# Optimization experiments

Measured on AMD Instinct MI355X. Metric: run time of the kernel, lower is better.

The kernel has to match this reference:

```python
import jax, jax.numpy as jnp
import numpy as np

NUM_ENT_CLASS = 150
NORMED_REL_VEC_DIST = False


def box_cxcywh_to_xyxy(b):
    cx, cy, w, h = b[..., 0], b[..., 1], b[..., 2], b[..., 3]
    return jnp.stack([cx - 0.5 * w, cy - 0.5 * h, cx + 0.5 * w, cy + 0.5 * h], axis=-1)


def box_xyxy_to_cxcywh(b):
    x0, y0, x1, y1 = b[..., 0], b[..., 1], b[..., 2], b[..., 3]
    return jnp.stack([(x0 + x1) * 0.5, (y0 + y1) * 0.5, x1 - x0, y1 - y0], axis=-1)


def generalized_box_iou(a, b):
    # a: [N,4], b: [M,4], xyxy -> [N,M]
    area_a = (a[:, 2] - a[:, 0]) * (a[:, 3] - a[:, 1])
    area_b = (b[:, 2] - b[:, 0]) * (b[:, 3] - b[:, 1])
    lt = jnp.maximum(a[:, None, :2], b[None, :, :2])
    rb = jnp.minimum(a[:, None, 2:], b[None, :, 2:])
    wh = jnp.clip(rb - lt, 0.0)
    inter = wh[..., 0] * wh[..., 1]
    union = area_a[:, None] + area_b[None, :] - inter
    iou = inter / union
    lt_c = jnp.minimum(a[:, None, :2], b[None, :, :2])
    rb_c = jnp.maximum(a[:, None, 2:], b[None, :, 2:])
    wh_c = jnp.clip(rb_c - lt_c, 0.0)
    area_c = wh_c[..., 0] * wh_c[..., 1]
    return iou - (area_c - union) / area_c


def cdist_l2(a, b):
    # a: [N,C], b: [M,C] -> [N,M] euclidean distance (gram-matrix form)
    d2 = (jnp.sum(a * a, -1)[:, None] + jnp.sum(b * b, -1)[None, :]
          - 2.0 * (a @ b.T))
    return jnp.sqrt(jnp.maximum(d2, 1e-12))


def _per_image(ent_box_n, ent_logits, ro_logits, rs_logits, ro_box_n, rs_box_n,
               rel_vec_n, scale):
    # scale: [4] = [w, h, w, h]
    ent_box = box_cxcywh_to_xyxy(ent_box_n) * scale[None, :]           # [Ne,4] pixels
    ent_cnter = box_xyxy_to_cxcywh(ent_box)[..., :2]                    # [Ne,2]
    ent_cnter_normed = ent_box_n[..., :2]

    # num_ent_class (150) != logits dim (151) -> softmax, drop background
    ro_dist = jax.nn.softmax(ro_logits, axis=-1)[..., :-1]              # [Nr,150]
    rs_dist = jax.nn.softmax(rs_logits, axis=-1)[..., :-1]
    ent_prob = jax.nn.softmax(ent_logits, axis=-1)[..., :-1]            # [Ne,150]
    ent_score = jnp.max(ent_prob, axis=-1)                              # [Ne]

    ro_box = box_cxcywh_to_xyxy(ro_box_n) * scale[None, :]              # [Nr,4]
    rs_box = box_cxcywh_to_xyxy(rs_box_n) * scale[None, :]
    rel_vec = rel_vec_n * scale[None, :]                                # [Nr,4]

    if NORMED_REL_VEC_DIST:
        vec, sc, oc = rel_vec_n, ent_cnter_normed, ent_cnter_normed
    else:
        vec, sc, oc = rel_vec, ent_cnter, ent_cnter

    # L1 distance of rel-vector endpoints to entity centers -> [Nr,Ne]
    dist_s = (jnp.abs(vec[:, None, 0] - sc[None, :, 0])
              + jnp.abs(vec[:, None, 1] - sc[None, :, 1]))
    dist_o = (jnp.abs(vec[:, None, 2] - oc[None, :, 0])
              + jnp.abs(vec[:, None, 3] - oc[None, :, 1]))
    match_vec_sub = 1.0 / (dist_s + 1.0)
    match_vec_obj = 1.0 / (dist_o + 1.0)

    m_s = ent_score[None, :] * match_vec_sub                            # conf-weighted
    m_o = ent_score[None, :] * match_vec_obj

    sub_giou = jnp.clip(generalized_box_iou(ent_box, rs_box), 0.0)      # [Ne,Nr]
    obj_giou = jnp.clip(generalized_box_iou(ent_box, ro_box), 0.0)

    sub_cls = 1.0 / (cdist_l2(rs_dist, ent_prob) + 1.0)                 # [Nr,Ne]
    obj_cls = 1.0 / (cdist_l2(ro_dist, ent_prob) + 1.0)

    dist_s_final = m_s * sub_cls * sub_giou.T                           # [Nr,Ne]
    dist_o_final = m_o * obj_cls * obj_giou.T
    return dist_s_final, dist_o_final


def setup_inputs() -> dict:
    key = jax.random.key(0)
    ks = jax.random.split(key, 8)
    B, Ne, Nr, C1 = 64, 500, 500, NUM_ENT_CLASS + 1
    inp = {
        "pred_boxes": jax.random.uniform(ks[0], (B, Ne, 4), jnp.float32),
        "pred_logits": jax.random.normal(ks[1], (B, Ne, C1), jnp.float32),
        "pred_rel_obj_logits": jax.random.normal(ks[2], (B, Nr, C1), jnp.float32),
        "pred_rel_sub_logits": jax.random.normal(ks[3], (B, Nr, C1), jnp.float32),
        "pred_rel_obj_box": jax.random.uniform(ks[4], (B, Nr, 4), jnp.float32),
        "pred_rel_sub_box": jax.random.uniform(ks[5], (B, Nr, 4), jnp.float32),
        "pred_rel_vec": jax.random.uniform(ks[6], (B, Nr, 4), jnp.float32),
        "target_sizes": 600.0 + 600.0 * jax.random.uniform(ks[7], (B, 2), jnp.float32),
    }
    return inp


def reference(pred_boxes, pred_logits, pred_rel_obj_logits, pred_rel_sub_logits,
              pred_rel_obj_box, pred_rel_sub_box, pred_rel_vec, target_sizes):
    img_h, img_w = target_sizes[:, 0], target_sizes[:, 1]
    scale_fct = jnp.stack([img_w, img_h, img_w, img_h], axis=1)  # [B,4]
    sub_dist, obj_dist = jax.vmap(_per_image)(
        pred_boxes, pred_logits, pred_rel_obj_logits, pred_rel_sub_logits,
        pred_rel_obj_box, pred_rel_sub_box, pred_rel_vec, scale_fct)
    return sub_dist, obj_dist
```

## Files before the change

kernel.cpp:

```cpp
#include <hip/hip_runtime.h>
#include <math.h>

#define NB   64
#define NPT  500
#define NPTP 512
#define C1   151
#define CM1  150
#define KP   160
#define EAF  12
#define RAF  20

typedef __bf16 bf16x8 __attribute__((ext_vector_type(8)));
typedef float  f32x4  __attribute__((ext_vector_type(4)));

__device__ __forceinline__ float rcpf(float x) { return __builtin_amdgcn_rcpf(x); }
__device__ __forceinline__ float rsqf(float x) { return __builtin_amdgcn_rsqf(x); }

extern "C" __global__ void __launch_bounds__(256)
k_pre(const float* __restrict__ boxes, const float* __restrict__ ent_logits,
      const float* __restrict__ ro_logits, const float* __restrict__ rs_logits,
      const float* __restrict__ ro_box, const float* __restrict__ rs_box,
      const float* __restrict__ rel_vec, const float* __restrict__ tsz,
      __bf16* __restrict__ entP, __bf16* __restrict__ rsP, __bf16* __restrict__ roP,
      float* __restrict__ entAux, float* __restrict__ relAux)
{
    const int w    = threadIdx.x >> 6;
    const int lane = threadIdx.x & 63;
    const int row  = blockIdx.x * 4 + w;
    const int set  = row / (NB * NPT);
    const int idx  = row - set * (NB * NPT);
    const int b    = idx / NPT;
    const int i    = idx - b * NPT;

    const float* src = (set == 0 ? ent_logits : (set == 1 ? rs_logits : ro_logits))
                       + (size_t)(b * NPT + i) * C1;

    const float x0 = src[lane];
    const float x1 = src[lane + 64];
    const float x2 = (lane < C1 - 128) ? src[lane + 128] : -INFINITY;

    float m = fmaxf(fmaxf(x0, x1), x2);
    #pragma unroll
    for (int off = 32; off; off >>= 1) m = fmaxf(m, __shfl_xor(m, off, 64));

    const float e0 = __expf(x0 - m);
    const float e1 = __expf(x1 - m);
    const float e2 = (lane < C1 - 128) ? __expf(x2 - m) : 0.f;
    float s = e0 + e1 + e2;
    #pragma unroll
    for (int off = 32; off; off >>= 1) s += __shfl_xor(s, off, 64);

    const float inv = 1.f / s;
    const float p0 = e0 * inv;
    const float p1 = e1 * inv;
    const float p2 = e2 * inv;

    __bf16* dst = (set == 0 ? entP : (set == 1 ? rsP : roP)) + ((size_t)b * NPTP + i) * KP;
    dst[lane]      = (__bf16)p0;
    dst[lane + 64] = (__bf16)p1;
    if (lane + 128 < KP)
        dst[lane + 128] = (lane + 128 < CM1) ? (__bf16)p2 : (__bf16)0.f;

    float pm = fmaxf(p0, p1);
    float nn = p0 * p0 + p1 * p1;
    if (lane + 128 < CM1) { pm = fmaxf(pm, p2); nn += p2 * p2; }
    #pragma unroll
    for (int off = 32; off; off >>= 1) {
        pm = fmaxf(pm, __shfl_xor(pm, off, 64));
        nn += __shfl_xor(nn, off, 64);
    }

    if (lane == 0) {
        const float hh = tsz[b * 2 + 0];
        const float ww = tsz[b * 2 + 1];
        if (set == 0) {
            const float* bb = boxes + (size_t)(b * NPT + i) * 4;
            const float cx = bb[0], cy = bb[1], bw = bb[2], bh = bb[3];
            const float X0 = (cx - 0.5f * bw) * ww, Y0 = (cy - 0.5f * bh) * hh;
            const float X1 = (cx + 0.5f * bw) * ww, Y1 = (cy + 0.5f * bh) * hh;
            float* A = entAux + (size_t)(b * NPT + i) * EAF;
            A[0] = pm;
            A[1] = 0.5f * (X0 + X1);
            A[2] = 0.5f * (Y0 + Y1);
            A[3] = nn;
            A[4] = X0; A[5] = Y0; A[6] = X1; A[7] = Y1;
            A[8] = (X1 - X0) * (Y1 - Y0);
        } else if (set == 1) {
            const float* bb = rs_box  + (size_t)(b * NPT + i) * 4;
            const float* vv = rel_vec + (size_t)(b * NPT + i) * 4;
            const float cx = bb[0], cy = bb[1], bw = bb[2], bh = bb[3];
            float* A = relAux + (size_t)(b * NPT + i) * RAF;
            const float X0 = (cx - 0.5f * bw) * ww, Y0 = (cy - 0.5f * bh) * hh;
            const float X1 = (cx + 0.5f * bw) * ww, Y1 = (cy + 0.5f * bh) * hh;
            A[0] = X0; A[1] = Y0; A[2] = X1; A[3] = Y1;
            A[8]  = vv[0] * ww; A[9]  = vv[1] * hh;
            A[10] = vv[2] * ww; A[11] = vv[3] * hh;
            A[12] = nn;
            A[14] = (X1 - X0) * (Y1 - Y0);
        } else {
            const float* bb = ro_box + (size_t)(b * NPT + i) * 4;
            const float cx = bb[0], cy = bb[1], bw = bb[2], bh = bb[3];
            float* A = relAux + (size_t)(b * NPT + i) * RAF;
            const float X0 = (cx - 0.5f * bw) * ww, Y0 = (cy - 0.5f * bh) * hh;
            const float X1 = (cx + 0.5f * bw) * ww, Y1 = (cy + 0.5f * bh) * hh;
            A[4] = X0; A[5] = Y0; A[6] = X1; A[7] = Y1;
            A[13] = nn;
            A[15] = (X1 - X0) * (Y1 - Y0);
        }
    }
}

template <bool FULL>
__device__ __forceinline__ void epilogue(
    const float (*eA)[EAF], const float (*rA)[RAF],
    const f32x4* accS, const f32x4* accO,
    int lr, int kq, int wv, int b, int e0T, int r0T,
    float* __restrict__ outS, float* __restrict__ outO)
{
    f32x4 ev0[4], ev1[4];
    float eArea[4];
    #pragma unroll
    for (int et = 0; et < 4; ++et) {
        const float* ep = eA[et * 16 + lr];
        ev0[et] = *(const f32x4*)(ep);
        ev1[et] = *(const f32x4*)(ep + 4);
        eArea[et] = ep[8];
    }

    const unsigned baseR0 = ((unsigned)b * NPT + (unsigned)(r0T + wv * 16 + kq * 4)) * NPT;
    const unsigned eBase  = (unsigned)(e0T + lr);

    #pragma unroll
    for (int reg = 0; reg < 4; ++reg) {
        const int rIdx = wv * 16 + kq * 4 + reg;
        const bool rOK = FULL || (r0T + rIdx < NPT);
        const float* rp = rA[rIdx];
        const f32x4 rsB = *(const f32x4*)(rp);
        const f32x4 roB = *(const f32x4*)(rp + 4);
        const f32x4 vv  = *(const f32x4*)(rp + 8);
        const f32x4 rn  = *(const f32x4*)(rp + 12);
        const unsigned rowOff = baseR0 + (unsigned)reg * NPT;

        #pragma unroll
        for (int et = 0; et < 4; ++et) {
            const float score = ev0[et][0], ecx = ev0[et][1], ecy = ev0[et][2], en2 = ev0[et][3];
            const float ex0 = ev1[et][0], ey0 = ev1[et][1], ex1 = ev1[et][2], ey1 = ev1[et][3];
            const float aE = eArea[et];

            const float iwS = fmaxf(fminf(ex1, rsB[2]) - fmaxf(ex0, rsB[0]), 0.f);
            const float ihS = fmaxf(fminf(ey1, rsB[3]) - fmaxf(ey0, rsB[1]), 0.f);
            const float inS = iwS * ihS;
            const float unS = aE + rn[2] - inS;
            const float aCS = (fmaxf(ex1, rsB[2]) - fminf(ex0, rsB[0]))
                            * (fmaxf(ey1, rsB[3]) - fminf(ey0, rsB[1]));
            const float gS  = fmaxf(fmaf(inS, rcpf(unS), fmaf(unS, rcpf(aCS), -1.f)), 0.f);

            const float iwO = fmaxf(fminf(ex1, roB[2]) - fmaxf(ex0, roB[0]), 0.f);
            const float ihO = fmaxf(fminf(ey1, roB[3]) - fmaxf(ey0, roB[1]), 0.f);
            const float inO = iwO * ihO;
            const float unO = aE + rn[3] - inO;
            const float aCO = (fmaxf(ex1, roB[2]) - fminf(ex0, roB[0]))
                            * (fmaxf(ey1, roB[3]) - fminf(ey0, roB[1]));
            const float gO  = fmaxf(fmaf(inO, rcpf(unO), fmaf(unO, rcpf(aCO), -1.f)), 0.f);

            const float d2s = fmaxf(fmaf(-2.f, accS[et][reg], rn[0] + en2), 1e-12f);
            const float d2o = fmaxf(fmaf(-2.f, accO[et][reg], rn[1] + en2), 1e-12f);
            const float dS  = d2s * rsqf(d2s);
            const float dO  = d2o * rsqf(d2o);
            const float distS = fabsf(vv[0] - ecx) + fabsf(vv[1] - ecy);
            const float distO = fabsf(vv[2] - ecx) + fabsf(vv[3] - ecy);
            const float qS = rcpf((distS + 1.f) * (dS + 1.f));
            const float qO = rcpf((distO + 1.f) * (dO + 1.f));

            const float vS = score * qS * gS;
            const float vO = score * qO * gO;

            const unsigned o = rowOff + eBase + (unsigned)(et * 16);
            if (FULL || (rOK && (int)(eBase + et * 16) < NPT)) {
                outS[o] = vS;
                outO[o] = vO;
            }
        }
    }
}

extern "C" __global__ void __launch_bounds__(256, 4)
k_main(const __bf16* __restrict__ entP, const __bf16* __restrict__ rsP,
       const __bf16* __restrict__ roP, const float* __restrict__ eAuxG,
       const float* __restrict__ rAuxG,
       float* __restrict__ outS, float* __restrict__ outO)
{
    __shared__ __align__(16) float eA[64][EAF];
    __shared__ __align__(16) float rA[64][RAF];

    const int tid = threadIdx.x;
    const int b   = blockIdx.z;
    const int e0T = blockIdx.x * 64;
    const int r0T = blockIdx.y * 64;

    {
        const float4 z = {0.f, 0.f, 0.f, 0.f};
        for (int t = tid; t < 64 * (EAF / 4); t += 256) {
            const int e = t / (EAF / 4), q = t % (EAF / 4);
            const int ge = e0T + e;
            ((float4*)eA[e])[q] = (ge < NPT)
                ? ((const float4*)(eAuxG + ((size_t)b * NPT + ge) * EAF))[q] : z;
        }
        for (int t = tid; t < 64 * (RAF / 4); t += 256) {
            const int r = t / (RAF / 4), q = t % (RAF / 4);
            const int gr = r0T + r;
            ((float4*)rA[r])[q] = (gr < NPT)
                ? ((const float4*)(rAuxG + ((size_t)b * NPT + gr) * RAF))[q] : z;
        }
    }
    __syncthreads();

    const int wv   = tid >> 6;
    const int lane = tid & 63;
    const int lr   = lane & 15;
    const int kq   = lane >> 4;

    const size_t bOff = (size_t)b * NPTP;
    const __bf16* rsRow = rsP  + (bOff + r0T + wv * 16 + lr) * KP;
    const __bf16* roRow = roP  + (bOff + r0T + wv * 16 + lr) * KP;
    const __bf16* enRow = entP + (bOff + e0T + lr) * KP;

    f32x4 accS[4] = {{0,0,0,0},{0,0,0,0},{0,0,0,0},{0,0,0,0}};
    f32x4 accO[4] = {{0,0,0,0},{0,0,0,0},{0,0,0,0},{0,0,0,0}};

    #pragma unroll
    for (int ks = 0; ks < 5; ++ks) {
        const int ko = ks * 32 + kq * 8;
        const bf16x8 ars = *(const bf16x8*)(rsRow + ko);
        const bf16x8 aro = *(const bf16x8*)(roRow + ko);
        #pragma unroll
        for (int et = 0; et < 4; ++et) {
            const bf16x8 be = *(const bf16x8*)(enRow + (size_t)et * 16 * KP + ko);
            accS[et] = __builtin_amdgcn_mfma_f32_16x16x32_bf16(ars, be, accS[et], 0, 0, 0);
            accO[et] = __builtin_amdgcn_mfma_f32_16x16x32_bf16(aro, be, accO[et], 0, 0, 0);
        }
    }

    if (e0T + 64 <= NPT && r0T + 64 <= NPT) {
        epilogue<true >(eA, rA, accS, accO, lr, kq, wv, b, e0T, r0T, outS, outO);
    } else {
        epilogue<false>(eA, rA, accS, accO, lr, kq, wv, b, e0T, r0T, outS, outO);
    }
}

extern "C" void kernel_launch(void* const* d_in, const int* in_sizes, int n_in,
                              void* d_out, int out_size, void* d_ws, size_t ws_size,
                              hipStream_t stream)
{
    const float* boxes      = (const float*)d_in[0];
    const float* ent_logits = (const float*)d_in[1];
    const float* ro_logits  = (const float*)d_in[2];
    const float* rs_logits  = (const float*)d_in[3];
    const float* ro_box     = (const float*)d_in[4];
    const float* rs_box     = (const float*)d_in[5];
    const float* rel_vec    = (const float*)d_in[6];
    const float* tsz        = (const float*)d_in[7];

    const size_t PROB_ELEMS = (size_t)NB * NPTP * KP;
    __bf16* entP = (__bf16*)d_ws;
    __bf16* rsP  = entP + PROB_ELEMS;
    __bf16* roP  = rsP  + PROB_ELEMS;
    float*  eAux = (float*)(roP + PROB_ELEMS);
    float*  rAux = eAux + (size_t)NB * NPT * EAF;

    float* outS = (float*)d_out;
    float* outO = outS + (size_t)NB * NPT * NPT;

    hipLaunchKernelGGL(k_pre, dim3(24000), dim3(256), 0, stream,
                       boxes, ent_logits, ro_logits, rs_logits,
                       ro_box, rs_box, rel_vec, tsz,
                       entP, rsP, roP, eAux, rAux);

    hipLaunchKernelGGL(k_main, dim3(8, 8, NB), dim3(256), 0, stream,
                       entP, rsP, roP, eAux, rAux, outS, outO);
}
```

Baseline: 276.0 us.

## Use 16-lane rows in softmax prep and MFMA-fragment probability layout

The prep kernel now handles one row per 16 lanes instead of per wavefront, which cuts the number of blocks and shuffle rounds. It computes the max probability and squared norm from the exp values, with no second reduction pass. Probabilities are written in a grouped layout that matches the MFMA operand fragments, so each lane's bf16x8 loads in the main kernel are contiguous across lanes. The main grid also puts the batch index first, likely to improve L2 locality between tiles of the same image. In exchange, the stores in the prep kernel become scattered 2-byte writes.

After: 235.7 us. 1.17x faster.

```diff
diff --git a/kernel.cpp b/kernel.cpp
--- a/kernel.cpp
+++ b/kernel.cpp
@@ -3,12 +3,14 @@
 
 #define NB   64
 #define NPT  500
-#define NPTP 512
 #define C1   151
 #define CM1  150
-#define KP   160
 #define EAF  12
 #define RAF  20
+
+#define GRP_ELEMS  2560
+#define IMG_ELEMS  (32 * GRP_ELEMS)
+#define PROB_ELEMS ((size_t)NB * IMG_ELEMS)
 
 typedef __bf16 bf16x8 __attribute__((ext_vector_type(8)));
 typedef float  f32x4  __attribute__((ext_vector_type(4)));
@@ -24,61 +26,76 @@
       __bf16* __restrict__ entP, __bf16* __restrict__ rsP, __bf16* __restrict__ roP,
       float* __restrict__ entAux, float* __restrict__ relAux)
 {
-    const int w    = threadIdx.x >> 6;
-    const int lane = threadIdx.x & 63;
-    const int row  = blockIdx.x * 4 + w;
-    const int set  = row / (NB * NPT);
-    const int idx  = row - set * (NB * NPT);
-    const int b    = idx / NPT;
-    const int i    = idx - b * NPT;
+    const int tid = threadIdx.x;
+    const int q   = tid & 15;
+    const int rl  = tid >> 4;
+    const int bx  = blockIdx.x;
+    const int set = bx / 2000;
+    const int rowIdx = (bx - set * 2000) * 16 + rl;
+    const int b = rowIdx / 500;
+    const int i = rowIdx - b * 500;
 
     const float* src = (set == 0 ? ent_logits : (set == 1 ? rs_logits : ro_logits))
-                       + (size_t)(b * NPT + i) * C1;
-
-    const float x0 = src[lane];
-    const float x1 = src[lane + 64];
-    const float x2 = (lane < C1 - 128) ? src[lane + 128] : -INFINITY;
-
-    float m = fmaxf(fmaxf(x0, x1), x2);
-    #pragma unroll
-    for (int off = 32; off; off >>= 1) m = fmaxf(m, __shfl_xor(m, off, 64));
-
-    const float e0 = __expf(x0 - m);
-    const float e1 = __expf(x1 - m);
-    const float e2 = (lane < C1 - 128) ? __expf(x2 - m) : 0.f;
-    float s = e0 + e1 + e2;
-    #pragma unroll
-    for (int off = 32; off; off >>= 1) s += __shfl_xor(s, off, 64);
-
-    const float inv = 1.f / s;
-    const float p0 = e0 * inv;
-    const float p1 = e1 * inv;
-    const float p2 = e2 * inv;
-
-    __bf16* dst = (set == 0 ? entP : (set == 1 ? rsP : roP)) + ((size_t)b * NPTP + i) * KP;
-    dst[lane]      = (__bf16)p0;
-    dst[lane + 64] = (__bf16)p1;
-    if (lane + 128 < KP)
-        dst[lane + 128] = (lane + 128 < CM1) ? (__bf16)p2 : (__bf16)0.f;
-
-    float pm = fmaxf(p0, p1);
-    float nn = p0 * p0 + p1 * p1;
-    if (lane + 128 < CM1) { pm = fmaxf(pm, p2); nn += p2 * p2; }
-    #pragma unroll
-    for (int off = 32; off; off >>= 1) {
-        pm = fmaxf(pm, __shfl_xor(pm, off, 64));
-        nn += __shfl_xor(nn, off, 64);
-    }
-
-    if (lane == 0) {
+                       + (size_t)rowIdx * C1;
+
+    float x[10];
+    #pragma unroll
+    for (int t = 0; t < 9; ++t) x[t] = src[q + 16 * t];
+    x[9] = (q <= 6) ? src[q + 144] : -INFINITY;
+
+    float mAll = x[0];
+    #pragma unroll
+    for (int t = 1; t < 10; ++t) mAll = fmaxf(mAll, x[t]);
+    float mKept = x[0];
+    #pragma unroll
+    for (int t = 1; t < 9; ++t) mKept = fmaxf(mKept, x[t]);
+    if (q <= 5) mKept = fmaxf(mKept, x[9]);
+
+    #pragma unroll
+    for (int off = 1; off < 16; off <<= 1) {
+        mAll  = fmaxf(mAll,  __shfl_xor(mAll,  off, 16));
+        mKept = fmaxf(mKept, __shfl_xor(mKept, off, 16));
+    }
+
+    float e[10], s = 0.f, s2 = 0.f;
+    #pragma unroll
+    for (int t = 0; t < 9; ++t) {
+        e[t] = __expf(x[t] - mAll);
+        s  += e[t];
+        s2 += e[t] * e[t];
+    }
+    e[9] = (q <= 6) ? __expf(x[9] - mAll) : 0.f;
+    s += e[9];
+    if (q <= 5) s2 += e[9] * e[9];
+
+    #pragma unroll
+    for (int off = 1; off < 16; off <<= 1) {
+        s  += __shfl_xor(s,  off, 16);
+        s2 += __shfl_xor(s2, off, 16);
+    }
+
+    const float inv = rcpf(s);
+    const float pm  = __expf(mKept - mAll) * inv;
+    const float nn  = s2 * inv * inv;
+
+    __bf16* dstT = (set == 0 ? entP : (set == 1 ? rsP : roP));
+    const int g  = i >> 4, ir = i & 15;
+    __bf16* dst = dstT + ((size_t)b * 32 + g) * GRP_ELEMS + ir * 8 + (q & 7);
+    const int qh = q >> 3;
+    #pragma unroll
+    for (int t = 0; t < 9; ++t)
+        dst[(2 * t + qh) * 128] = (__bf16)(e[t] * inv);
+    dst[(18 + qh) * 128] = (q <= 5) ? (__bf16)(e[9] * inv) : (__bf16)0.f;
+
+    if (q == 0) {
         const float hh = tsz[b * 2 + 0];
         const float ww = tsz[b * 2 + 1];
         if (set == 0) {
-            const float* bb = boxes + (size_t)(b * NPT + i) * 4;
+            const float* bb = boxes + (size_t)rowIdx * 4;
             const float cx = bb[0], cy = bb[1], bw = bb[2], bh = bb[3];
             const float X0 = (cx - 0.5f * bw) * ww, Y0 = (cy - 0.5f * bh) * hh;
             const float X1 = (cx + 0.5f * bw) * ww, Y1 = (cy + 0.5f * bh) * hh;
-            float* A = entAux + (size_t)(b * NPT + i) * EAF;
+            float* A = entAux + (size_t)rowIdx * EAF;
             A[0] = pm;
             A[1] = 0.5f * (X0 + X1);
             A[2] = 0.5f * (Y0 + Y1);
@@ -86,10 +103,10 @@
             A[4] = X0; A[5] = Y0; A[6] = X1; A[7] = Y1;
             A[8] = (X1 - X0) * (Y1 - Y0);
         } else if (set == 1) {
-            const float* bb = rs_box  + (size_t)(b * NPT + i) * 4;
-            const float* vv = rel_vec + (size_t)(b * NPT + i) * 4;
+            const float* bb = rs_box  + (size_t)rowIdx * 4;
+            const float* vv = rel_vec + (size_t)rowIdx * 4;
             const float cx = bb[0], cy = bb[1], bw = bb[2], bh = bb[3];
-            float* A = relAux + (size_t)(b * NPT + i) * RAF;
+            float* A = relAux + (size_t)rowIdx * RAF;
             const float X0 = (cx - 0.5f * bw) * ww, Y0 = (cy - 0.5f * bh) * hh;
             const float X1 = (cx + 0.5f * bw) * ww, Y1 = (cy + 0.5f * bh) * hh;
             A[0] = X0; A[1] = Y0; A[2] = X1; A[3] = Y1;
@@ -98,9 +115,9 @@
             A[12] = nn;
             A[14] = (X1 - X0) * (Y1 - Y0);
         } else {
-            const float* bb = ro_box + (size_t)(b * NPT + i) * 4;
+            const float* bb = ro_box + (size_t)rowIdx * 4;
             const float cx = bb[0], cy = bb[1], bw = bb[2], bh = bb[3];
-            float* A = relAux + (size_t)(b * NPT + i) * RAF;
+            float* A = relAux + (size_t)rowIdx * RAF;
             const float X0 = (cx - 0.5f * bw) * ww, Y0 = (cy - 0.5f * bh) * hh;
             const float X1 = (cx + 0.5f * bw) * ww, Y1 = (cy + 0.5f * bh) * hh;
             A[4] = X0; A[5] = Y0; A[6] = X1; A[7] = Y1;
@@ -194,23 +211,23 @@
     __shared__ __align__(16) float rA[64][RAF];
 
     const int tid = threadIdx.x;
-    const int b   = blockIdx.z;
-    const int e0T = blockIdx.x * 64;
-    const int r0T = blockIdx.y * 64;
+    const int b   = blockIdx.x;
+    const int e0T = (blockIdx.y & 7) * 64;
+    const int r0T = (blockIdx.y >> 3) * 64;
 
     {
         const float4 z = {0.f, 0.f, 0.f, 0.f};
         for (int t = tid; t < 64 * (EAF / 4); t += 256) {
-            const int e = t / (EAF / 4), q = t % (EAF / 4);
+            const int e = t / (EAF / 4), qq = t % (EAF / 4);
             const int ge = e0T + e;
-            ((float4*)eA[e])[q] = (ge < NPT)
-                ? ((const float4*)(eAuxG + ((size_t)b * NPT + ge) * EAF))[q] : z;
+            ((float4*)eA[e])[qq] = (ge < NPT)
+                ? ((const float4*)(eAuxG + ((size_t)b * NPT + ge) * EAF))[qq] : z;
         }
         for (int t = tid; t < 64 * (RAF / 4); t += 256) {
-            const int r = t / (RAF / 4), q = t % (RAF / 4);
+            const int r = t / (RAF / 4), qq = t % (RAF / 4);
             const int gr = r0T + r;
-            ((float4*)rA[r])[q] = (gr < NPT)
-                ? ((const float4*)(rAuxG + ((size_t)b * NPT + gr) * RAF))[q] : z;
+            ((float4*)rA[r])[qq] = (gr < NPT)
+                ? ((const float4*)(rAuxG + ((size_t)b * NPT + gr) * RAF))[qq] : z;
         }
     }
     __syncthreads();
@@ -220,22 +237,23 @@
     const int lr   = lane & 15;
     const int kq   = lane >> 4;
 
-    const size_t bOff = (size_t)b * NPTP;
-    const __bf16* rsRow = rsP  + (bOff + r0T + wv * 16 + lr) * KP;
-    const __bf16* roRow = roP  + (bOff + r0T + wv * 16 + lr) * KP;
-    const __bf16* enRow = entP + (bOff + e0T + lr) * KP;
+    const int gR = (r0T >> 4) + wv;
+    const int gE = (e0T >> 4);
+    const __bf16* rsBase = rsP  + ((size_t)b * 32 + gR) * GRP_ELEMS + lr * 8;
+    const __bf16* roBase = roP  + ((size_t)b * 32 + gR) * GRP_ELEMS + lr * 8;
+    const __bf16* enBase = entP + ((size_t)b * 32 + gE) * GRP_ELEMS + lr * 8;
 
     f32x4 accS[4] = {{0,0,0,0},{0,0,0,0},{0,0,0,0},{0,0,0,0}};
     f32x4 accO[4] = {{0,0,0,0},{0,0,0,0},{0,0,0,0},{0,0,0,0}};
 
     #pragma unroll
     for (int ks = 0; ks < 5; ++ks) {
-        const int ko = ks * 32 + kq * 8;
-        const bf16x8 ars = *(const bf16x8*)(rsRow + ko);
-        const bf16x8 aro = *(const bf16x8*)(roRow + ko);
+        const int kOff = (ks * 4 + kq) * 128;
+        const bf16x8 ars = *(const bf16x8*)(rsBase + kOff);
+        const bf16x8 aro = *(const bf16x8*)(roBase + kOff);
         #pragma unroll
         for (int et = 0; et < 4; ++et) {
-            const bf16x8 be = *(const bf16x8*)(enRow + (size_t)et * 16 * KP + ko);
+            const bf16x8 be = *(const bf16x8*)(enBase + et * GRP_ELEMS + kOff);
             accS[et] = __builtin_amdgcn_mfma_f32_16x16x32_bf16(ars, be, accS[et], 0, 0, 0);
             accO[et] = __builtin_amdgcn_mfma_f32_16x16x32_bf16(aro, be, accO[et], 0, 0, 0);
         }
@@ -261,7 +279,6 @@
     const float* rel_vec    = (const float*)d_in[6];
     const float* tsz        = (const float*)d_in[7];
 
-    const size_t PROB_ELEMS = (size_t)NB * NPTP * KP;
     __bf16* entP = (__bf16*)d_ws;
     __bf16* rsP  = entP + PROB_ELEMS;
     __bf16* roP  = rsP  + PROB_ELEMS;
@@ -271,11 +288,11 @@
     float* outS = (float*)d_out;
     float* outO = outS + (size_t)NB * NPT * NPT;
 
-    hipLaunchKernelGGL(k_pre, dim3(24000), dim3(256), 0, stream,
+    hipLaunchKernelGGL(k_pre, dim3(6000), dim3(256), 0, stream,
                        boxes, ent_logits, ro_logits, rs_logits,
                        ro_box, rs_box, rel_vec, tsz,
                        entP, rsP, roP, eAux, rAux);
 
-    hipLaunchKernelGGL(k_main, dim3(8, 8, NB), dim3(256), 0, stream,
+    hipLaunchKernelGGL(k_main, dim3(64, 64), dim3(256), 0, stream,
                        entP, rsP, roP, eAux, rAux, outS, outO);
 }
```
